# Performance work log

Hardware: AMD Instinct MI355X
Metric: run time of the kernel (lower is better)

Reference implementation:

```python
import jax, jax.numpy as jnp
import numpy as np

B, T, D = 4, 2048, 2048
H = 16
KD = D // 2          # key_dim = expand_k * d_model
VD = D               # value_dim = expand_v * d_model
DK = KD // H         # head_k_dim = 64
DV = VD // H         # head_v_dim = 128
LR = 16              # gate_low_rank_dim
EPS = 1e-5
GATE_LOGIT_NORMALIZER = 16.0


def setup_inputs() -> dict:
    key = jax.random.key(0)
    ks = jax.random.split(key, 9)
    def w(k, shape):
        fan_in = shape[0]
        return (jax.random.normal(k, shape, jnp.float32) * (fan_in ** -0.5)).astype(jnp.float32)
    return {
        "x":      jax.random.normal(ks[0], (B, T, D), jnp.float32),
        "Wq":     w(ks[1], (D, KD)),
        "Wk":     w(ks[2], (D, KD)),
        "Wv":     w(ks[3], (D, VD)),
        "Wg":     w(ks[4], (D, VD)),      # output gate projection
        "Wgk1":   w(ks[5], (D, LR)),      # gk low-rank down-proj (no bias)
        "Wgk2":   w(ks[6], (LR, KD)),     # gk up-proj
        "bgk2":   jnp.zeros((KD,), jnp.float32),
        "norm_w": jnp.ones((DV,), jnp.float32),  # per-head RMSNorm weight
        "Wo":     w(ks[7], (VD, D)),
    }


def reference(x, Wq, Wk, Wv, Wg, Wgk1, Wgk2, bgk2, norm_w, Wo):
    b, t, _ = x.shape
    dv = norm_w.shape[0]
    vd = Wv.shape[1]
    h = vd // dv
    dk = Wq.shape[1] // h
    scale = dk ** -0.5

    q = (x @ Wq).reshape(b, t, h, dk) * scale
    k = (x @ Wk).reshape(b, t, h, dk)
    v = (x @ Wv).reshape(b, t, h, dv)
    # forget gate: logsigmoid(low_rank_proj(x)) / gate_logit_normalizer
    gk = jax.nn.log_sigmoid((x @ Wgk1) @ Wgk2 + bgk2) / GATE_LOGIT_NORMALIZER
    gk = gk.reshape(b, t, h, dk)

    # time-major for scan: [T, B, H, d]
    qT = jnp.moveaxis(q, 1, 0)
    kT = jnp.moveaxis(k, 1, 0)
    vT = jnp.moveaxis(v, 1, 0)
    gT = jnp.moveaxis(gk, 1, 0)

    def step(S, inp):
        qt, kt, vt, gt = inp
        # S_t = diag(exp(gk_t)) S_{t-1} + k_t^T v_t ; shape [B,H,DK,DV]
        S = S * jnp.exp(gt)[..., None] + kt[..., None] * vt[..., None, :]
        ot = jnp.einsum('bhk,bhkv->bhv', qt, S)
        return S, ot

    S0 = jnp.zeros((b, h, dk, dv), x.dtype)
    _, o = jax.lax.scan(step, S0, (qT, kT, vT, gT))
    o = jnp.moveaxis(o, 0, 1)  # [B, T, H, DV]

    # FusedRMSNormSwishGate: rmsnorm(o) * weight * swish(g), per head dim
    g = (x @ Wg).reshape(b, t, h, dv)
    o = o * jax.lax.rsqrt(jnp.mean(o * o, axis=-1, keepdims=True) + EPS) * norm_w
    o = o * (g * jax.nn.sigmoid(g))
    return o.reshape(b, t, vd) @ Wo
```

## Files before the change

kernel.cpp:

```cpp
#include <hip/hip_runtime.h>
#include <hip/hip_bf16.h>
#include <type_traits>


using bf16x8 = __attribute__((ext_vector_type(8))) short;
using f32x4  = __attribute__((ext_vector_type(4))) float;
using f32x16 = __attribute__((ext_vector_type(16))) float;

static __device__ __forceinline__ float bf2f(ushort u) {
  union { unsigned int i; float f; } v;
  v.i = ((unsigned int)u) << 16;
  return v.f;
}
static __device__ __forceinline__ ushort f2bf(float f) {
  __hip_bfloat16 h = __float2bfloat16(f);
  return *reinterpret_cast<ushort*>(&h);
}
static __device__ __forceinline__ unsigned int pack2(float lo, float hi) {
  return (unsigned int)f2bf(lo) | ((unsigned int)f2bf(hi) << 16);
}
static __device__ __forceinline__ void unpack8(uint4 v, float* f) {
  f[0] = bf2f((ushort)(v.x & 0xffff)); f[1] = bf2f((ushort)(v.x >> 16));
  f[2] = bf2f((ushort)(v.y & 0xffff)); f[3] = bf2f((ushort)(v.y >> 16));
  f[4] = bf2f((ushort)(v.z & 0xffff)); f[5] = bf2f((ushort)(v.z >> 16));
  f[6] = bf2f((ushort)(v.w & 0xffff)); f[7] = bf2f((ushort)(v.w >> 16));
}

#define GLDS16(g, l) __builtin_amdgcn_global_load_lds( \
    (const __attribute__((address_space(1))) unsigned int*)(g), \
    (__attribute__((address_space(3))) unsigned int*)(l), 16, 0, 0)

#define SWZ3(row) ((((row) & 1) << 2) | (((row) >> 1) & 3))

__global__ __launch_bounds__(256) void f32_to_bf16(
    const float* __restrict__ in, ushort* __restrict__ out, long n) {
  long i = ((long)blockIdx.x * 256 + threadIdx.x) * 8;
  if (i >= n) return;
  float4 a = *(const float4*)(in + i);
  float4 b = *(const float4*)(in + i + 4);
  uint4 o;
  o.x = pack2(a.x, a.y); o.y = pack2(a.z, a.w);
  o.z = pack2(b.x, b.y); o.w = pack2(b.z, b.w);
  *(uint4*)(out + i) = o;
}

__global__ __launch_bounds__(256) void transpose_f32_bf16(
    const float* __restrict__ in, ushort* __restrict__ out, int R, int C) {
  __shared__ float tile[64][65];
  const int t = threadIdx.x;
  const int tc = blockIdx.x * 64;
  const int tr = blockIdx.y * 64;
  const int lr = t >> 2;
  const int lc = (t & 3) * 16;
  const float* ip = in + (long)(tr + lr) * C + tc + lc;
#pragma unroll
  for (int j = 0; j < 4; ++j)
    *(float4*)(&tile[lr][lc + j * 4]) = *(const float4*)(ip + j * 4);
  __syncthreads();
  const int c = t >> 2;
  const int r0 = (t & 3) * 16;
  ushort tmp[16];
#pragma unroll
  for (int j = 0; j < 16; ++j) tmp[j] = f2bf(tile[r0 + j][c]);
  ushort* op = out + (long)(tc + c) * R + tr + r0;
  *(uint4*)(op)     = *(uint4*)(tmp);
  *(uint4*)(op + 8) = *(uint4*)(tmp + 8);
}

template <typename OT>
__global__ __launch_bounds__(512, 2) void gemm_bt8(
    const ushort* __restrict__ A, const ushort* __restrict__ BT,
    OT* __restrict__ C, int M, int N, int K) {
  __shared__ ushort sA[2 * 16384];
  __shared__ ushort sB[2 * 16384];
  const int t = threadIdx.x;
  const int nbx = N >> 8;
  const int cpx = gridDim.x >> 3;
  const int wg = ((int)blockIdx.x & 7) * cpx + ((int)blockIdx.x >> 3);
  const int brow = (wg / nbx) * 256;
  const int bcol = (wg % nbx) * 256;

  const int w = t >> 6, l = t & 63;
  const int wm = w >> 2, wn = w & 3;
  const int l31 = l & 31, l5 = l >> 5;
  const int NT = K >> 6;

  const int srow = t >> 3;
  const int cswz = ((t & 7) ^ SWZ3(srow)) * 8;
  const ushort* Abase = A + (size_t)(brow + srow) * K + cswz;
  const ushort* Bbase = BT + (size_t)(bcol + srow) * K + cswz;
  const int t8 = t * 8;

  auto stageA = [&](int bb, int hh, int jt) {
    const ushort* s = Abase + (size_t)(hh * 128) * K + jt * 64;
    ushort* d = sA + bb * 16384 + hh * 8192 + t8;
    GLDS16(s, d);
    GLDS16(s + (size_t)64 * K, d + 4096);
  };
  auto stageB = [&](int bb, int hh, int jt) {
    const ushort* s = Bbase + (size_t)(hh * 128) * K + jt * 64;
    ushort* d = sB + bb * 16384 + hh * 8192 + t8;
    GLDS16(s, d);
    GLDS16(s + (size_t)64 * K, d + 4096);
  };

  const int swz = SWZ3(l31 & 7);
  const int aRow = (wm * 32 + l31) * 64;
  const int bRow = (wn * 32 + l31) * 64;
#define KSL(ks) ((((ks) * 2 + l5) ^ swz) * 8)

  f32x16 acc[4][2];
#pragma unroll
  for (int m = 0; m < 4; ++m)
#pragma unroll
    for (int n = 0; n < 2; ++n)
#pragma unroll
      for (int r = 0; r < 16; ++r) acc[m][n][r] = 0.f;

  stageA(0, 0, 0); stageB(0, 0, 0); stageB(0, 1, 0); stageA(0, 1, 0);
  stageA(1, 0, 1); stageB(1, 0, 1); stageB(1, 1, 1);
  asm volatile("s_waitcnt vmcnt(6)" ::: "memory");
  __builtin_amdgcn_s_barrier();

  for (int kt = 0; kt < NT; ++kt) {
    const int bb = kt & 1;
    const int off = bb * 16384;
    bf16x8 aF[2][4], bF[2][4];

    if (kt + 1 < NT) stageA(bb ^ 1, 1, kt + 1);
#pragma unroll
    for (int mf = 0; mf < 2; ++mf)
#pragma unroll
      for (int ks = 0; ks < 4; ++ks)
        aF[mf][ks] = *(const bf16x8*)(sA + off + mf * 4096 + aRow + KSL(ks));
#pragma unroll
    for (int nh = 0; nh < 2; ++nh)
#pragma unroll
      for (int ks = 0; ks < 4; ++ks)
        bF[nh][ks] = *(const bf16x8*)(sB + off + nh * 8192 + bRow + KSL(ks));
    __builtin_amdgcn_s_setprio(1);
#pragma unroll
    for (int mf = 0; mf < 2; ++mf)
#pragma unroll
      for (int ks = 0; ks < 4; ++ks)
        acc[mf][0] = __builtin_amdgcn_mfma_f32_32x32x16_bf16(aF[mf][ks], bF[0][ks], acc[mf][0], 0, 0, 0);
#pragma unroll
    for (int mf = 0; mf < 2; ++mf)
#pragma unroll
      for (int ks = 0; ks < 4; ++ks)
        acc[mf][1] = __builtin_amdgcn_mfma_f32_32x32x16_bf16(aF[mf][ks], bF[1][ks], acc[mf][1], 0, 0, 0);
    __builtin_amdgcn_s_setprio(0);
    __builtin_amdgcn_s_barrier();

    if (kt + 2 < NT) { stageA(bb, 0, kt + 2); stageB(bb, 0, kt + 2); stageB(bb, 1, kt + 2); }
#pragma unroll
    for (int mf = 0; mf < 2; ++mf)
#pragma unroll
      for (int ks = 0; ks < 4; ++ks)
        aF[mf][ks] = *(const bf16x8*)(sA + off + 8192 + mf * 4096 + aRow + KSL(ks));
    __builtin_amdgcn_s_setprio(1);
#pragma unroll
    for (int mf = 0; mf < 2; ++mf)
#pragma unroll
      for (int ks = 0; ks < 4; ++ks)
        acc[2 + mf][0] = __builtin_amdgcn_mfma_f32_32x32x16_bf16(aF[mf][ks], bF[0][ks], acc[2 + mf][0], 0, 0, 0);
#pragma unroll
    for (int mf = 0; mf < 2; ++mf)
#pragma unroll
      for (int ks = 0; ks < 4; ++ks)
        acc[2 + mf][1] = __builtin_amdgcn_mfma_f32_32x32x16_bf16(aF[mf][ks], bF[1][ks], acc[2 + mf][1], 0, 0, 0);
    __builtin_amdgcn_s_setprio(0);
    if (kt < NT - 2)       asm volatile("s_waitcnt vmcnt(6)" ::: "memory");
    else if (kt == NT - 2) asm volatile("s_waitcnt vmcnt(0)" ::: "memory");
    __builtin_amdgcn_s_barrier();
  }
#undef KSL

#pragma unroll
  for (int mf = 0; mf < 4; ++mf)
#pragma unroll
    for (int nf = 0; nf < 2; ++nf) {
      long col = bcol + nf * 128 + wn * 32 + l31;
      long rbase = brow + mf * 64 + wm * 32 + 4 * l5;
#pragma unroll
      for (int r = 0; r < 16; ++r) {
        long row = rbase + (r & 3) + 8 * (r >> 2);
        if constexpr (std::is_same_v<OT, ushort>) C[row * N + col] = f2bf(acc[mf][nf][r]);
        else                                      C[row * N + col] = acc[mf][nf][r];
      }
    }
}

__global__ __launch_bounds__(256) void gate_kernel(
    const ushort* __restrict__ xb, const float* __restrict__ Wgk1,
    const float* __restrict__ Wgk2, const float* __restrict__ bgk2,
    ushort* __restrict__ gbuf) {
  const long m0 = (long)blockIdx.x * 8;
  const int t = threadIdx.x;
  __shared__ float sx[8][2048];
  __shared__ float red[16][8][16];
  __shared__ float z1[8][16];
#pragma unroll
  for (int u = 0; u < 8; ++u) {
    int idx = (u * 256 + t) * 8;
    int r = idx >> 11, cc = idx & 2047;
    uint4 v = *(const uint4*)(xb + (m0 + r) * 2048 + cc);
    float f[8];
    unpack8(v, f);
    *(float4*)(&sx[r][cc])     = (float4){f[0], f[1], f[2], f[3]};
    *(float4*)(&sx[r][cc + 4]) = (float4){f[4], f[5], f[6], f[7]};
  }
  __syncthreads();
  const int j = t & 15, dg = t >> 4;
  float a8[8] = {0.f, 0.f, 0.f, 0.f, 0.f, 0.f, 0.f, 0.f};
  const float* wp = Wgk1 + (dg * 128) * 16 + j;
  for (int dc = 0; dc < 128; dc += 4) {
    float w0 = wp[(dc + 0) * 16], w1 = wp[(dc + 1) * 16];
    float w2 = wp[(dc + 2) * 16], w3 = wp[(dc + 3) * 16];
    const int dd = dg * 128 + dc;
#pragma unroll
    for (int r = 0; r < 8; ++r) {
      float4 xv = *(const float4*)(&sx[r][dd]);
      a8[r] += xv.x * w0 + xv.y * w1 + xv.z * w2 + xv.w * w3;
    }
  }
#pragma unroll
  for (int r = 0; r < 8; ++r) red[dg][r][j] = a8[r];
  __syncthreads();
  if (t < 128) {
    int r = t >> 4, jj = t & 15;
    float s = 0.f;
#pragma unroll
    for (int g = 0; g < 16; ++g) s += red[g][r][jj];
    z1[r][jj] = s;
  }
  __syncthreads();
#pragma unroll
  for (int q = 0; q < 4; ++q) {
    int n = q * 256 + t;
    float w2v[16];
#pragma unroll
    for (int l2 = 0; l2 < 16; ++l2) w2v[l2] = Wgk2[l2 * 1024 + n];
    float bb = bgk2[n];
#pragma unroll
    for (int r = 0; r < 8; ++r) {
      float a = bb;
#pragma unroll
      for (int l2 = 0; l2 < 16; ++l2) a += z1[r][l2] * w2v[l2];
      float ls = fminf(a, 0.f) - log1pf(__expf(-fabsf(a)));
      gbuf[(m0 + r) * 1024 + n] = f2bf(ls * 0.0625f);
    }
  }
}

__global__ __launch_bounds__(256) void chunk_contrib_kernel(
    const ushort* __restrict__ qkvg, const ushort* __restrict__ gbuf,
    ushort* __restrict__ STbuf, float* __restrict__ EGtot) {
  const int blk = blockIdx.x;
  const int bh = blk >> 5, c = blk & 31;
  const int b = bh >> 4, h = bh & 15;
  const long row0 = (long)b * 2048 + c * 64;
  const int th = threadIdx.x;

  __shared__ float  gc[64][65];
  __shared__ ushort khT[64][72];
  __shared__ ushort vT[128][72];

  {
    const int t = th >> 2;
    const int k0 = (th & 3) * 16;
    const ushort* gp = gbuf + (row0 + t) * 1024 + h * 64 + k0;
    uint4 a = *(const uint4*)gp;
    uint4 b4 = *(const uint4*)(gp + 8);
    float f[8];
    unpack8(a, f);
#pragma unroll
    for (int j = 0; j < 8; ++j) gc[t][k0 + j] = f[j];
    unpack8(b4, f);
#pragma unroll
    for (int j = 0; j < 8; ++j) gc[t][k0 + 8 + j] = f[j];
  }
  __syncthreads();
  if (th < 64) {
    float s = 0.f;
    for (int t = 0; t < 64; ++t) { s += gc[t][th]; gc[t][th] = s; }
  }
  __syncthreads();
  if (th < 64) EGtot[(long)blk * 64 + th] = __expf(gc[63][th]);

  {
    const int s = th & 63, kq = th >> 6;
    const ushort* kp = qkvg + (row0 + s) * 6144 + 1024 + h * 64 + kq * 16;
    uint4 a = *(const uint4*)kp;
    uint4 b4 = *(const uint4*)(kp + 8);
    float f[16];
    unpack8(a, f); unpack8(b4, f + 8);
#pragma unroll
    for (int j = 0; j < 16; ++j) {
      int k = kq * 16 + j;
      khT[k][s] = f2bf(f[j] * __expf(gc[63][k] - gc[s][k]));
    }
    const ushort* vp = qkvg + (row0 + s) * 6144 + 2048 + h * 128 + kq * 32;
#pragma unroll
    for (int u = 0; u < 4; ++u) {
      uint4 vv = *(const uint4*)(vp + u * 8);
      const ushort* pv = (const ushort*)&vv;
#pragma unroll
      for (int j = 0; j < 8; ++j) vT[kq * 32 + u * 8 + j][s] = pv[j];
    }
  }
  __syncthreads();

  const int w = th >> 6, l = th & 63;
  const int lr = l & 15, kq8 = (l >> 4) * 8;
  f32x4 acc[4][2];
#pragma unroll
  for (int m = 0; m < 4; ++m)
#pragma unroll
    for (int n = 0; n < 2; ++n) acc[m][n] = (f32x4){0.f, 0.f, 0.f, 0.f};
#pragma unroll
  for (int ks = 0; ks < 64; ks += 32) {
#pragma unroll
    for (int m = 0; m < 4; ++m) {
      bf16x8 af = *(const bf16x8*)(&khT[m * 16 + lr][ks + kq8]);
#pragma unroll
      for (int n = 0; n < 2; ++n) {
        bf16x8 bv = *(const bf16x8*)(&vT[w * 32 + n * 16 + lr][ks + kq8]);
        acc[m][n] = __builtin_amdgcn_mfma_f32_16x16x32_bf16(af, bv, acc[m][n], 0, 0, 0);
      }
    }
  }
  ushort* Cc = STbuf + (long)blk * 8192;
  const int rq = (l >> 4) * 4;
#pragma unroll
  for (int m = 0; m < 4; ++m)
#pragma unroll
    for (int n = 0; n < 2; ++n) {
      int dv = w * 32 + n * 16 + lr;
      ushort tmp[4];
#pragma unroll
      for (int r = 0; r < 4; ++r) tmp[r] = f2bf(acc[m][n][r]);
      *(uint2*)(Cc + dv * 64 + m * 16 + rq) = *(uint2*)tmp;
    }
}

__global__ __launch_bounds__(256) void chunk_scan_kernel(
    ushort* __restrict__ STbuf, const float* __restrict__ EGtot) {
  const int blk = blockIdx.x;
  const int bh = blk >> 2, qd = blk & 3;
  const int th = threadIdx.x;
  const int dv = qd * 32 + (th >> 3);
  const int k0 = (th & 7) * 8;
  ushort* base = STbuf + (long)bh * 32 * 8192 + dv * 64 + k0;
  const float* eg = EGtot + (long)bh * 32 * 64 + k0;
  float S[8];
#pragma unroll
  for (int i = 0; i < 8; ++i) S[i] = 0.f;
  uint4 cv = *(const uint4*)base;
  float4 e0 = *(const float4*)(eg);
  float4 e1 = *(const float4*)(eg + 4);
  for (int c = 0; c < 32; ++c) {
    ushort* cur = base;
    base += 8192; eg += 64;
    uint4 nv = cv; float4 n0 = e0, n1 = e1;
    if (c < 31) {
      nv = *(const uint4*)base;
      n0 = *(const float4*)(eg);
      n1 = *(const float4*)(eg + 4);
    }
    float cf[8];
    unpack8(cv, cf);
    float ee[8] = {e0.x, e0.y, e0.z, e0.w, e1.x, e1.y, e1.z, e1.w};
    ushort so[8];
#pragma unroll
    for (int i = 0; i < 8; ++i) {
      so[i] = f2bf(S[i]);
      S[i] = S[i] * ee[i] + cf[i];
    }
    *(uint4*)cur = *(uint4*)so;
    cv = nv; e0 = n0; e1 = n1;
  }
}

__global__ __launch_bounds__(256) void chunk_output_kernel(
    const ushort* __restrict__ qkvg, const ushort* __restrict__ gbuf,
    const ushort* __restrict__ STbuf, const float* __restrict__ norm_w,
    ushort* __restrict__ oo) {
  const int blk = blockIdx.x;
  const int bh = blk >> 5, c = blk & 31;
  const int b = bh >> 4, h = bh & 15;
  const long row0 = (long)b * 2048 + c * 64;
  const int th = threadIdx.x;

  __shared__ __align__(16) char pool[71936];
  float  (*gc)[65]  = (float(*)[65])(pool);
  ushort (*qg)[72]  = (ushort(*)[72])(pool + 16640);
  ushort (*kg)[72]  = (ushort(*)[72])(pool + 25856);
  ushort (*vT)[72]  = (ushort(*)[72])(pool + 35072);
  ushort (*STs)[72] = (ushort(*)[72])(pool + 53504);
  ushort (*P)[72]   = (ushort(*)[72])(pool);

  {
    const int t = th >> 2;
    const int k0 = (th & 3) * 16;
    const ushort* gp = gbuf + (row0 + t) * 1024 + h * 64 + k0;
    uint4 a = *(const uint4*)gp;
    uint4 b4 = *(const uint4*)(gp + 8);
    float f[8];
    unpack8(a, f);
#pragma unroll
    for (int j = 0; j < 8; ++j) gc[t][k0 + j] = f[j];
    unpack8(b4, f);
#pragma unroll
    for (int j = 0; j < 8; ++j) gc[t][k0 + 8 + j] = f[j];

    const ushort* qp = qkvg + (row0 + t) * 6144 + h * 64 + k0;
    *(uint4*)(&qg[t][k0])     = *(const uint4*)qp;
    *(uint4*)(&qg[t][k0 + 8]) = *(const uint4*)(qp + 8);
    const ushort* kp = qp + 1024;
    *(uint4*)(&kg[t][k0])     = *(const uint4*)kp;
    *(uint4*)(&kg[t][k0 + 8]) = *(const uint4*)(kp + 8);
  }
  {
    const int s = th & 63, kq = th >> 6;
    const ushort* vp = qkvg + (row0 + s) * 6144 + 2048 + h * 128 + kq * 32;
#pragma unroll
    for (int u = 0; u < 4; ++u) {
      uint4 vv = *(const uint4*)(vp + u * 8);
      const ushort* pv = (const ushort*)&vv;
#pragma unroll
      for (int j = 0; j < 8; ++j) vT[kq * 32 + u * 8 + j][s] = pv[j];
    }
  }
  {
    const int row = th >> 1;
    const int col0 = (th & 1) * 32;
    const ushort* sp = STbuf + (long)blk * 8192 + row * 64 + col0;
#pragma unroll
    for (int u = 0; u < 4; ++u)
      *(uint4*)(&STs[row][col0 + u * 8]) = *(const uint4*)(sp + u * 8);
  }
  __syncthreads();
  if (th < 64) {
    float s = 0.f;
    for (int t = 0; t < 64; ++t) { s += gc[t][th]; gc[t][th] = s; }
  }
  __syncthreads();
  {
    const int t = th & 63, kb = (th >> 6) * 16;
#pragma unroll
    for (int u = 0; u < 2; ++u) {
      uint4 qv = *(const uint4*)(&qg[t][kb + u * 8]);
      uint4 kv = *(const uint4*)(&kg[t][kb + u * 8]);
      float qf[8], kf[8];
      unpack8(qv, qf); unpack8(kv, kf);
      ushort qo[8], ko[8];
#pragma unroll
      for (int j = 0; j < 8; ++j) {
        float g = gc[t][kb + u * 8 + j];
        qo[j] = f2bf(qf[j] * __expf(g) * 0.125f);
        ko[j] = f2bf(kf[j] * __expf(-g));
      }
      *(uint4*)(&qg[t][kb + u * 8]) = *(uint4*)qo;
      *(uint4*)(&kg[t][kb + u * 8]) = *(uint4*)ko;
    }
  }
  __syncthreads();

  const int w = th >> 6, l = th & 63;
  const int lr = l & 15, kq8 = (l >> 4) * 8;
  const int rq = (l >> 4) * 4;

  f32x4 acc1[4];
#pragma unroll
  for (int n = 0; n < 4; ++n) acc1[n] = (f32x4){0.f, 0.f, 0.f, 0.f};
#pragma unroll
  for (int kk = 0; kk < 64; kk += 32) {
    bf16x8 af = *(const bf16x8*)(&qg[w * 16 + lr][kk + kq8]);
#pragma unroll
    for (int n = 0; n < 4; ++n) {
      bf16x8 bv = *(const bf16x8*)(&kg[n * 16 + lr][kk + kq8]);
      acc1[n] = __builtin_amdgcn_mfma_f32_16x16x32_bf16(af, bv, acc1[n], 0, 0, 0);
    }
  }
#pragma unroll
  for (int n = 0; n < 4; ++n) {
    int s = n * 16 + lr;
#pragma unroll
    for (int r = 0; r < 4; ++r) {
      int t = w * 16 + rq + r;
      P[t][s] = f2bf(s <= t ? acc1[n][r] : 0.f);
    }
  }
  __syncthreads();

  f32x4 acc2[8];
#pragma unroll
  for (int n = 0; n < 8; ++n) acc2[n] = (f32x4){0.f, 0.f, 0.f, 0.f};
#pragma unroll
  for (int ks = 0; ks < 64; ks += 32) {
    bf16x8 af = *(const bf16x8*)(&P[w * 16 + lr][ks + kq8]);
#pragma unroll
    for (int n = 0; n < 8; ++n) {
      bf16x8 bv = *(const bf16x8*)(&vT[n * 16 + lr][ks + kq8]);
      acc2[n] = __builtin_amdgcn_mfma_f32_16x16x32_bf16(af, bv, acc2[n], 0, 0, 0);
    }
  }
#pragma unroll
  for (int kk = 0; kk < 64; kk += 32) {
    bf16x8 af = *(const bf16x8*)(&qg[w * 16 + lr][kk + kq8]);
#pragma unroll
    for (int n = 0; n < 8; ++n) {
      bf16x8 bv = *(const bf16x8*)(&STs[n * 16 + lr][kk + kq8]);
      acc2[n] = __builtin_amdgcn_mfma_f32_16x16x32_bf16(af, bv, acc2[n], 0, 0, 0);
    }
  }

  float gv[8][4];
#pragma unroll
  for (int n = 0; n < 8; ++n) {
    int dv = n * 16 + lr;
#pragma unroll
    for (int r = 0; r < 4; ++r)
      gv[n][r] = bf2f(qkvg[(row0 + w * 16 + rq + r) * 6144 + 4096 + h * 128 + dv]);
  }

  float sumsq[4] = {0.f, 0.f, 0.f, 0.f};
#pragma unroll
  for (int n = 0; n < 8; ++n)
#pragma unroll
    for (int r = 0; r < 4; ++r) sumsq[r] += acc2[n][r] * acc2[n][r];
#pragma unroll
  for (int d = 1; d < 16; d <<= 1)
#pragma unroll
    for (int r = 0; r < 4; ++r) sumsq[r] += __shfl_xor(sumsq[r], d);
  float inv[4];
#pragma unroll
  for (int r = 0; r < 4; ++r) inv[r] = rsqrtf(sumsq[r] * (1.f / 128.f) + 1e-5f);

#pragma unroll
  for (int n = 0; n < 8; ++n) {
    int dv = n * 16 + lr;
    float nw = norm_w[dv];
#pragma unroll
    for (int r = 0; r < 4; ++r) {
      float g = gv[n][r];
      float sw = g / (1.f + __expf(-g));
      oo[(row0 + w * 16 + rq + r) * 2048 + h * 128 + dv] =
          f2bf(acc2[n][r] * inv[r] * nw * sw);
    }
  }
}

extern "C" void kernel_launch(void* const* d_in, const int* in_sizes, int n_in,
                              void* d_out, int out_size, void* d_ws, size_t ws_size,
                              hipStream_t stream) {
  const float* x      = (const float*)d_in[0];
  const float* Wq     = (const float*)d_in[1];
  const float* Wk     = (const float*)d_in[2];
  const float* Wv     = (const float*)d_in[3];
  const float* Wg     = (const float*)d_in[4];
  const float* Wgk1   = (const float*)d_in[5];
  const float* Wgk2   = (const float*)d_in[6];
  const float* bgk2   = (const float*)d_in[7];
  const float* norm_w = (const float*)d_in[8];
  const float* Wo     = (const float*)d_in[9];
  float* out = (float*)d_out;

  char* ws = (char*)d_ws;
  ushort* WT    = (ushort*)(ws);
  ushort* WoT   = (ushort*)(ws + 25165824);
  ushort* qkvg  = (ushort*)(ws + 33554432);
  ushort* gbuf  = (ushort*)(ws + 134217728);
  ushort* STbuf = (ushort*)(ws + 150994944);
  ushort* xb    = (ushort*)(ws + 150994944);
  float*  EGtot = (float*)(ws + 184549376);
  ushort* oo    = (ushort*)(ws + 185073664);

  dim3 blk(256);
  f32_to_bf16<<<dim3(8192), blk, 0, stream>>>(x, xb, (long)8192 * 2048);
  transpose_f32_bf16<<<dim3(16, 32), blk, 0, stream>>>(Wq, WT, 2048, 1024);
  transpose_f32_bf16<<<dim3(16, 32), blk, 0, stream>>>(Wk, WT + (size_t)1024 * 2048, 2048, 1024);
  transpose_f32_bf16<<<dim3(32, 32), blk, 0, stream>>>(Wv, WT + (size_t)2048 * 2048, 2048, 2048);
  transpose_f32_bf16<<<dim3(32, 32), blk, 0, stream>>>(Wg, WT + (size_t)4096 * 2048, 2048, 2048);
  transpose_f32_bf16<<<dim3(32, 32), blk, 0, stream>>>(Wo, WoT, 2048, 2048);

  gemm_bt8<ushort><<<dim3(768), dim3(512), 0, stream>>>(xb, WT, qkvg, 8192, 6144, 2048);
  gate_kernel<<<dim3(1024), blk, 0, stream>>>(xb, Wgk1, Wgk2, bgk2, gbuf);

  chunk_contrib_kernel<<<dim3(2048), blk, 0, stream>>>(qkvg, gbuf, STbuf, EGtot);
  chunk_scan_kernel<<<dim3(256), blk, 0, stream>>>(STbuf, EGtot);
  chunk_output_kernel<<<dim3(2048), blk, 0, stream>>>(qkvg, gbuf, STbuf, norm_w, oo);

  gemm_bt8<float><<<dim3(256), dim3(512), 0, stream>>>(oo, WoT, out, 8192, 2048, 2048);
}
```

Baseline: 485.0 us.

## Interleave GEMM LDS reads and global staging per quarter; parallelize gate cumsum

The GEMM main loop is split into four phases. Each phase loads only the fragments it needs from LDS and issues one slice of the next tile's global-to-LDS staging, with barriers between phases, so memory traffic overlaps more evenly with MFMA work. The per-chunk gate cumulative sum now runs on all 256 threads as four 16-step segments plus an offset fix-up, replacing the 64-step serial loop on 64 threads. The cost is extra barriers per iteration and a changed vmcnt accounting that must still match the new staging order.

```diff
diff --git a/kernel.cpp b/kernel.cpp
--- a/kernel.cpp
+++ b/kernel.cpp
@@ -31,6 +31,27 @@
     (__attribute__((address_space(3))) unsigned int*)(l), 16, 0, 0)
 
 #define SWZ3(row) ((((row) & 1) << 2) | (((row) >> 1) & 3))
+
+#define GC_CUMSUM(gc, th)                                              \
+  {                                                                    \
+    const int k_ = (th) & 63, seg_ = (th) >> 6;                        \
+    float s_ = 0.f;                                                    \
+    _Pragma("unroll")                                                  \
+    for (int i_ = 0; i_ < 16; ++i_) {                                  \
+      s_ += gc[seg_ * 16 + i_][k_];                                    \
+      gc[seg_ * 16 + i_][k_] = s_;                                     \
+    }                                                                  \
+    __syncthreads();                                                   \
+    float t0_ = gc[15][k_], t1_ = gc[31][k_], t2_ = gc[47][k_];        \
+    __syncthreads();                                                   \
+    float off_ = (seg_ > 0 ? t0_ : 0.f) + (seg_ > 1 ? t1_ : 0.f) +     \
+                 (seg_ > 2 ? t2_ : 0.f);                               \
+    if (seg_) {                                                        \
+      _Pragma("unroll")                                                \
+      for (int i_ = 0; i_ < 16; ++i_) gc[seg_ * 16 + i_][k_] += off_;  \
+    }                                                                  \
+    __syncthreads();                                                   \
+  }
 
 __global__ __launch_bounds__(256) void f32_to_bf16(
     const float* __restrict__ in, ushort* __restrict__ out, long n) {
@@ -118,32 +139,41 @@
       for (int r = 0; r < 16; ++r) acc[m][n][r] = 0.f;
 
   stageA(0, 0, 0); stageB(0, 0, 0); stageB(0, 1, 0); stageA(0, 1, 0);
+  asm volatile("s_waitcnt vmcnt(4)" ::: "memory");
   stageA(1, 0, 1); stageB(1, 0, 1); stageB(1, 1, 1);
   asm volatile("s_waitcnt vmcnt(6)" ::: "memory");
   __builtin_amdgcn_s_barrier();
 
   for (int kt = 0; kt < NT; ++kt) {
     const int bb = kt & 1;
-    const int off = bb * 16384;
+    const int aOff = bb * 16384, bOff = bb * 16384;
     bf16x8 aF[2][4], bF[2][4];
 
+#pragma unroll
+    for (int mf = 0; mf < 2; ++mf)
+#pragma unroll
+      for (int ks = 0; ks < 4; ++ks)
+        aF[mf][ks] = *(const bf16x8*)(sA + aOff + mf * 4096 + aRow + KSL(ks));
+#pragma unroll
+    for (int ks = 0; ks < 4; ++ks)
+      bF[0][ks] = *(const bf16x8*)(sB + bOff + bRow + KSL(ks));
     if (kt + 1 < NT) stageA(bb ^ 1, 1, kt + 1);
-#pragma unroll
-    for (int mf = 0; mf < 2; ++mf)
-#pragma unroll
-      for (int ks = 0; ks < 4; ++ks)
-        aF[mf][ks] = *(const bf16x8*)(sA + off + mf * 4096 + aRow + KSL(ks));
-#pragma unroll
-    for (int nh = 0; nh < 2; ++nh)
-#pragma unroll
-      for (int ks = 0; ks < 4; ++ks)
-        bF[nh][ks] = *(const bf16x8*)(sB + off + nh * 8192 + bRow + KSL(ks));
+    __builtin_amdgcn_s_barrier();
     __builtin_amdgcn_s_setprio(1);
 #pragma unroll
     for (int mf = 0; mf < 2; ++mf)
 #pragma unroll
       for (int ks = 0; ks < 4; ++ks)
         acc[mf][0] = __builtin_amdgcn_mfma_f32_32x32x16_bf16(aF[mf][ks], bF[0][ks], acc[mf][0], 0, 0, 0);
+    __builtin_amdgcn_s_setprio(0);
+    __builtin_amdgcn_s_barrier();
+
+#pragma unroll
+    for (int ks = 0; ks < 4; ++ks)
+      bF[1][ks] = *(const bf16x8*)(sB + bOff + 8192 + bRow + KSL(ks));
+    if (kt + 2 < NT) stageA(bb, 0, kt + 2);
+    __builtin_amdgcn_s_barrier();
+    __builtin_amdgcn_s_setprio(1);
 #pragma unroll
     for (int mf = 0; mf < 2; ++mf)
 #pragma unroll
@@ -152,18 +182,25 @@
     __builtin_amdgcn_s_setprio(0);
     __builtin_amdgcn_s_barrier();
 
-    if (kt + 2 < NT) { stageA(bb, 0, kt + 2); stageB(bb, 0, kt + 2); stageB(bb, 1, kt + 2); }
 #pragma unroll
     for (int mf = 0; mf < 2; ++mf)
 #pragma unroll
       for (int ks = 0; ks < 4; ++ks)
-        aF[mf][ks] = *(const bf16x8*)(sA + off + 8192 + mf * 4096 + aRow + KSL(ks));
+        aF[mf][ks] = *(const bf16x8*)(sA + aOff + 8192 + mf * 4096 + aRow + KSL(ks));
+    if (kt + 2 < NT) stageB(bb, 0, kt + 2);
+    __builtin_amdgcn_s_barrier();
     __builtin_amdgcn_s_setprio(1);
 #pragma unroll
     for (int mf = 0; mf < 2; ++mf)
 #pragma unroll
       for (int ks = 0; ks < 4; ++ks)
         acc[2 + mf][0] = __builtin_amdgcn_mfma_f32_32x32x16_bf16(aF[mf][ks], bF[0][ks], acc[2 + mf][0], 0, 0, 0);
+    __builtin_amdgcn_s_setprio(0);
+    __builtin_amdgcn_s_barrier();
+
+    if (kt + 2 < NT) stageB(bb, 1, kt + 2);
+    __builtin_amdgcn_s_barrier();
+    __builtin_amdgcn_s_setprio(1);
 #pragma unroll
     for (int mf = 0; mf < 2; ++mf)
 #pragma unroll
@@ -281,11 +318,7 @@
     for (int j = 0; j < 8; ++j) gc[t][k0 + 8 + j] = f[j];
   }
   __syncthreads();
-  if (th < 64) {
-    float s = 0.f;
-    for (int t = 0; t < 64; ++t) { s += gc[t][th]; gc[t][th] = s; }
-  }
-  __syncthreads();
+  GC_CUMSUM(gc, th)
   if (th < 64) EGtot[(long)blk * 64 + th] = __expf(gc[63][th]);
 
   {
@@ -441,11 +474,7 @@
       *(uint4*)(&STs[row][col0 + u * 8]) = *(const uint4*)(sp + u * 8);
   }
   __syncthreads();
-  if (th < 64) {
-    float s = 0.f;
-    for (int t = 0; t < 64; ++t) { s += gc[t][th]; gc[t][th] = s; }
-  }
-  __syncthreads();
+  GC_CUMSUM(gc, th)
   {
     const int t = th & 63, kb = (th >> 6) * 16;
 #pragma unroll
```

Result: faster. 464.7 us (-4.2%).
